# Kernel optimization log

Hardware: AMD Instinct MI355X
Metric: run time of the kernel (lower is better)

The kernel has to match this reference:

```python
import jax, jax.numpy as jnp
import numpy as np

D = 9  # nodefeat_n1 = 3 (resnet feat) + 6 (pos)


def _lstm_scan(x, Wih, Whh, bih, bhh, reverse=False):
    # x: [T, B, D] -> hidden states [T, B, D]; torch gate order i,f,g,o
    B = x.shape[1]
    def step(carry, xt):
        h, c = carry
        g = xt @ Wih.T + bih + h @ Whh.T + bhh
        i = jax.nn.sigmoid(g[:, :D])
        f = jax.nn.sigmoid(g[:, D:2*D])
        gg = jnp.tanh(g[:, 2*D:3*D])
        o = jax.nn.sigmoid(g[:, 3*D:])
        c = f * c + i * gg
        h = o * jnp.tanh(c)
        return (h, c), h
    init = (jnp.zeros((B, D), x.dtype), jnp.zeros((B, D), x.dtype))
    _, hs = jax.lax.scan(step, init, x, reverse=reverse)
    return hs


def _forward(nodes_feature, pos, attmat, msg_W, msg_b, gru_Wih, gru_Whh, gru_bih, gru_bhh,
             ro1_W, ro1_b, ro2_W, ro2_b, lf_Wih, lf_Whh, lf_bih, lf_bhh,
             lb_Wih, lb_Whh, lb_bih, lb_bhh, lr1_W, lr1_b, lr2_W, lr2_b, num_rec):
    node_feat = jnp.concatenate([nodes_feature, pos], axis=-1)  # [N,T,M,D]
    N, T, M, _ = node_feat.shape
    # valid_node_num = num_rec[b, 0] in the original code
    valid = (jnp.arange(M)[None, :] < num_rec[:, 0:1]).astype(node_feat.dtype)  # [N,M]
    att = attmat * valid[:, None, None, :]  # zero out invalid source nodes q
    src = node_feat  # message sources (h_w)
    hv = node_feat   # GRU hidden (h_v)
    hidden = node_feat
    for _ in range(2):  # iterN = 2 message-passing rounds
        msg = src @ msg_W.T + msg_b                    # [N,T,M,D] message_fc
        m = jnp.einsum('btnq,btqd->btnd', att, msg)    # attention-weighted sum over q
        # single-step GRU cell (torch gate order r,z,n)
        gx = m @ gru_Wih.T + gru_bih
        gh = hv @ gru_Whh.T + gru_bhh
        r = jax.nn.sigmoid(gx[..., :D] + gh[..., :D])
        z = jax.nn.sigmoid(gx[..., D:2*D] + gh[..., D:2*D])
        n = jnp.tanh(gx[..., 2*D:] + r * gh[..., 2*D:])
        h_new = (1.0 - z) * n + z * hv
        hidden = h_new * valid[:, None, :, None]       # invalid nodes never updated -> stay zero
        src = hidden
        hv = hidden
    vmask = valid[:, None, :, None]
    # per-frame readout (pred_label0)
    p0 = jax.nn.relu(hidden @ ro1_W.T + ro1_b) @ ro2_W.T + ro2_b
    pred_label0 = p0 * vmask
    # bidirectional LSTM over time, batched over (batch, node)
    x = hidden.transpose(1, 0, 2, 3).reshape(T, N * M, D)  # [T, N*M, D]
    hf = _lstm_scan(x, lf_Wih, lf_Whh, lf_bih, lf_bhh, reverse=False)
    hb = _lstm_scan(x, lb_Wih, lb_Whh, lb_bih, lb_bhh, reverse=True)
    out = jnp.concatenate([hf, hb], axis=-1).reshape(T, N, M, 2 * D).transpose(1, 0, 2, 3)
    p = jax.nn.relu(out @ lr1_W.T + lr1_b) @ lr2_W.T + lr2_b
    pred_label = p * vmask
    return pred_label, pred_label0


def setup_inputs() -> dict:
    key = jax.random.key(0)
    ks = jax.random.split(key, 32)
    N, T, M = 8192, 20, 6
    def u(k, shape, fan_in):
        s = 1.0 / np.sqrt(fan_in).astype(np.float32)
        return jax.random.uniform(k, shape, jnp.float32, -s, s)
    return {
        "nodes_feature": jax.random.normal(ks[0], (N, T, M, 3), jnp.float32),
        "pos": jax.random.normal(ks[1], (N, T, M, 6), jnp.float32),
        "attmat": jax.random.uniform(ks[2], (N, T, M, M), jnp.float32),
        "msg_W": u(ks[3], (D, D), D), "msg_b": u(ks[4], (D,), D),
        "gru_Wih": u(ks[5], (3 * D, D), D), "gru_Whh": u(ks[6], (3 * D, D), D),
        "gru_bih": u(ks[7], (3 * D,), D), "gru_bhh": u(ks[8], (3 * D,), D),
        "ro1_W": u(ks[9], (D, D), D), "ro1_b": u(ks[10], (D,), D),
        "ro2_W": u(ks[11], (7, D), D), "ro2_b": u(ks[12], (7,), D),
        "lf_Wih": u(ks[13], (4 * D, D), D), "lf_Whh": u(ks[14], (4 * D, D), D),
        "lf_bih": u(ks[15], (4 * D,), D), "lf_bhh": u(ks[16], (4 * D,), D),
        "lb_Wih": u(ks[17], (4 * D, D), D), "lb_Whh": u(ks[18], (4 * D, D), D),
        "lb_bih": u(ks[19], (4 * D,), D), "lb_bhh": u(ks[20], (4 * D,), D),
        "lr1_W": u(ks[21], (D, 2 * D), 2 * D), "lr1_b": u(ks[22], (D,), 2 * D),
        "lr2_W": u(ks[23], (7, D), D), "lr2_b": u(ks[24], (7,), D),
        "num_rec": jax.random.randint(ks[25], (N, T), 1, M + 1),
    }


def reference(nodes_feature, pos, attmat, msg_W, msg_b, gru_Wih, gru_Whh, gru_bih, gru_bhh,
              ro1_W, ro1_b, ro2_W, ro2_b, lf_Wih, lf_Whh, lf_bih, lf_bhh,
              lb_Wih, lb_Whh, lb_bih, lb_bhh, lr1_W, lr1_b, lr2_W, lr2_b, num_rec):
    return _forward(nodes_feature, pos, attmat, msg_W, msg_b, gru_Wih, gru_Whh, gru_bih, gru_bhh,
                    ro1_W, ro1_b, ro2_W, ro2_b, lf_Wih, lf_Whh, lf_bih, lf_bhh,
                    lb_Wih, lb_Whh, lb_bih, lb_bhh, lr1_W, lr1_b, lr2_W, lr2_b, num_rec)
```

## Files before the change

kernel.cpp:

```cpp
#include <hip/hip_runtime.h>

#define N_    8192
#define T_    20
#define M_    6
#define D_    9
#define NM_   (N_*M_)
#define NT_   (N_*T_)
#define NTM7_ (N_*T_*M_*7)

#define LOG2E 1.44269504088896f

__device__ __forceinline__ float sigm(float x){
    return __builtin_amdgcn_rcpf(1.f + __builtin_amdgcn_exp2f(-LOG2E * x));
}
__device__ __forceinline__ float tanh_(float x){
    return fmaf(2.f, __builtin_amdgcn_rcpf(1.f + __builtin_amdgcn_exp2f(-2.f*LOG2E * x)), -1.f);
}
__device__ __forceinline__ float shfl_(float v, int src){ return __shfl(v, src, 64); }

__global__ __launch_bounds__(256) void k_gnn(
    const float* __restrict__ nf,
    const float* __restrict__ pos,
    const float* __restrict__ am,
    const float* __restrict__ msgW, const float* __restrict__ msgb,
    const float* __restrict__ gWih, const float* __restrict__ gWhh,
    const float* __restrict__ gbih, const float* __restrict__ gbhh,
    const float* __restrict__ ro1W, const float* __restrict__ ro1b,
    const float* __restrict__ ro2W, const float* __restrict__ ro2b,
    const int*   __restrict__ numrec,
    float* __restrict__ hid,
    float* __restrict__ out0)
{
    const int lane = threadIdx.x & 63;
    const int wib  = threadIdx.x >> 6;
    const int g    = lane / 6;
    const int i    = lane - g * 6;
    const int gbase = g * 6;
    const bool lactive = (lane < 60);

    int ntIdx = (blockIdx.x * 4 + wib) * 10 + g;
    const bool active = lactive && (ntIdx < NT_);
    const int nt = active ? ntIdx : 0;
    const int n  = nt / T_;
    const int t  = nt - n * T_;

    float s[D_];
    {
        const float* p = nf + (size_t)nt * 18 + i * 3;
        s[0] = p[0]; s[1] = p[1]; s[2] = p[2];
    }
    {
        const float* p = pos + (size_t)nt * 36 + i * 6;
        #pragma unroll
        for (int k = 0; k < 6; ++k) s[3 + k] = p[k];
    }
    float attr[M_];
    {
        const float* p = am + (size_t)nt * 36 + i * 6;
        #pragma unroll
        for (int q = 0; q < M_; ++q) attr[q] = p[q];
    }
    const int nr = numrec[n * T_];
    #pragma unroll
    for (int q = 0; q < M_; ++q) attr[q] *= (q < nr) ? 1.f : 0.f;
    const float vmi = (i < nr) ? 1.f : 0.f;

    #pragma unroll
    for (int it = 0; it < 2; ++it) {
        float msg[D_];
        #pragma unroll
        for (int d = 0; d < D_; ++d) {
            float a = msgb[d];
            #pragma unroll
            for (int k = 0; k < D_; ++k) a += s[k] * msgW[d*9 + k];
            msg[d] = a;
        }
        float mm[D_];
        #pragma unroll
        for (int d = 0; d < D_; ++d) {
            float a = 0.f;
            #pragma unroll
            for (int q = 0; q < M_; ++q) a += attr[q] * shfl_(msg[d], gbase + q);
            mm[d] = a;
        }
        float gx[27], gh[27];
        #pragma unroll
        for (int j = 0; j < 27; ++j) {
            float ax = gbih[j], ah = gbhh[j];
            #pragma unroll
            for (int k = 0; k < D_; ++k) {
                ax += mm[k] * gWih[j*9 + k];
                ah += s[k]  * gWhh[j*9 + k];
            }
            gx[j] = ax; gh[j] = ah;
        }
        #pragma unroll
        for (int d = 0; d < D_; ++d) {
            float r  = sigm(gx[d]       + gh[d]);
            float z  = sigm(gx[9 + d]   + gh[9 + d]);
            float nn = tanh_(gx[18 + d] + r * gh[18 + d]);
            s[d] = vmi * ((1.f - z) * nn + z * s[d]);
        }
    }

    if (active) {
        float* hp = hid + (size_t)(n * M_ + i) * (T_ * D_) + t * D_;
        #pragma unroll
        for (int d = 0; d < D_; ++d) hp[d] = s[d];
    }

    float q9[D_];
    #pragma unroll
    for (int d = 0; d < D_; ++d) {
        float a = ro1b[d];
        #pragma unroll
        for (int k = 0; k < D_; ++k) a += s[k] * ro1W[d*9 + k];
        q9[d] = fmaxf(a, 0.f);
    }
    if (active) {
        float* op = out0 + (size_t)nt * 42 + i * 7;
        #pragma unroll
        for (int j = 0; j < 7; ++j) {
            float a = ro2b[j];
            #pragma unroll
            for (int k = 0; k < D_; ++k) a += q9[k] * ro2W[j*9 + k];
            op[j] = a * vmi;
        }
    }
}

#define CPB 14

__global__ __launch_bounds__(128) void k_lstm(
    const float* __restrict__ hid,
    const float* __restrict__ fWih, const float* __restrict__ fWhh,
    const float* __restrict__ fbih, const float* __restrict__ fbhh,
    const float* __restrict__ bWih, const float* __restrict__ bWhh,
    const float* __restrict__ bbih, const float* __restrict__ bbhh,
    const float* __restrict__ lr1W, const float* __restrict__ lr1b,
    const float* __restrict__ lr2W, const float* __restrict__ lr2b,
    const int*   __restrict__ numrec,
    float* __restrict__ out)
{
    __shared__ float hst[16 * 404];
    __shared__ float hxs[16 * 20];

    const int lane = threadIdx.x & 63;
    const int wib  = threadIdx.x >> 6;
    const int grp0 = lane / 9;
    const int d    = lane - grp0 * 9;
    const int row  = wib * 8 + grp0;
    const int grp  = (grp0 < 7) ? grp0 : 6;

    bool active = (lane < 63);
    int ci = blockIdx.x * CPB + wib * 7 + grp;
    active = active && (ci < NM_);
    const int nm = active ? ci : 0;

    const float* xb = hid + (size_t)nm * (T_ * D_);
    const int crow = row * 20;
    const int hrow = row * 404;

    {
        float wxi[9], wxf[9], wxg[9], wxo[9], whi[9], whf[9], whg[9], who[9];
        #pragma unroll
        for (int k = 0; k < 9; ++k) {
            wxi[k] = fWih[(d     )*9 + k];  whi[k] = fWhh[(d     )*9 + k];
            wxf[k] = fWih[(9  + d)*9 + k];  whf[k] = fWhh[(9  + d)*9 + k];
            wxg[k] = fWih[(18 + d)*9 + k];  whg[k] = fWhh[(18 + d)*9 + k];
            wxo[k] = fWih[(27 + d)*9 + k];  who[k] = fWhh[(27 + d)*9 + k];
        }
        const float bi = fbih[d]      + fbhh[d];
        const float bf = fbih[9 + d]  + fbhh[9 + d];
        const float bg = fbih[18 + d] + fbhh[18 + d];
        const float bo = fbih[27 + d] + fbhh[27 + d];

        hxs[crow + 2*d] = 0.f;
        float h = 0.f, c = 0.f;
        for (int t = 0; t < T_; ++t) {
            hxs[crow + 2*d + 1] = xb[t*9 + d];
            float gi = bi, gf = bf, gg = bg, go = bo;
            #pragma unroll
            for (int j = 0; j < 8; j += 2) {
                float4 v = *(const float4*)&hxs[crow + 2*j];
                gi = fmaf(v.x, whi[j], fmaf(v.y, wxi[j], gi));
                gf = fmaf(v.x, whf[j], fmaf(v.y, wxf[j], gf));
                gg = fmaf(v.x, whg[j], fmaf(v.y, wxg[j], gg));
                go = fmaf(v.x, who[j], fmaf(v.y, wxo[j], go));
                gi = fmaf(v.z, whi[j+1], fmaf(v.w, wxi[j+1], gi));
                gf = fmaf(v.z, whf[j+1], fmaf(v.w, wxf[j+1], gf));
                gg = fmaf(v.z, whg[j+1], fmaf(v.w, wxg[j+1], gg));
                go = fmaf(v.z, who[j+1], fmaf(v.w, wxo[j+1], go));
            }
            {
                float2 v = *(const float2*)&hxs[crow + 16];
                gi = fmaf(v.x, whi[8], fmaf(v.y, wxi[8], gi));
                gf = fmaf(v.x, whf[8], fmaf(v.y, wxf[8], gf));
                gg = fmaf(v.x, whg[8], fmaf(v.y, wxg[8], gg));
                go = fmaf(v.x, who[8], fmaf(v.y, wxo[8], go));
            }
            c = sigm(gf) * c + sigm(gi) * tanh_(gg);
            h = sigm(go) * tanh_(c);
            hst[hrow + t*20 + d] = h;
            hxs[crow + 2*d] = h;
        }
    }

    {
        float wxi[9], wxf[9], wxg[9], wxo[9], whi[9], whf[9], whg[9], who[9];
        #pragma unroll
        for (int k = 0; k < 9; ++k) {
            wxi[k] = bWih[(d     )*9 + k];  whi[k] = bWhh[(d     )*9 + k];
            wxf[k] = bWih[(9  + d)*9 + k];  whf[k] = bWhh[(9  + d)*9 + k];
            wxg[k] = bWih[(18 + d)*9 + k];  whg[k] = bWhh[(18 + d)*9 + k];
            wxo[k] = bWih[(27 + d)*9 + k];  who[k] = bWhh[(27 + d)*9 + k];
        }
        const float bi = bbih[d]      + bbhh[d];
        const float bf = bbih[9 + d]  + bbhh[9 + d];
        const float bg = bbih[18 + d] + bbhh[18 + d];
        const float bo = bbih[27 + d] + bbhh[27 + d];

        hxs[crow + 2*d] = 0.f;
        float h = 0.f, c = 0.f;
        for (int tt = T_ - 1; tt >= 0; --tt) {
            hxs[crow + 2*d + 1] = xb[tt*9 + d];
            float gi = bi, gf = bf, gg = bg, go = bo;
            #pragma unroll
            for (int j = 0; j < 8; j += 2) {
                float4 v = *(const float4*)&hxs[crow + 2*j];
                gi = fmaf(v.x, whi[j], fmaf(v.y, wxi[j], gi));
                gf = fmaf(v.x, whf[j], fmaf(v.y, wxf[j], gf));
                gg = fmaf(v.x, whg[j], fmaf(v.y, wxg[j], gg));
                go = fmaf(v.x, who[j], fmaf(v.y, wxo[j], go));
                gi = fmaf(v.z, whi[j+1], fmaf(v.w, wxi[j+1], gi));
                gf = fmaf(v.z, whf[j+1], fmaf(v.w, wxf[j+1], gf));
                gg = fmaf(v.z, whg[j+1], fmaf(v.w, wxg[j+1], gg));
                go = fmaf(v.z, who[j+1], fmaf(v.w, wxo[j+1], go));
            }
            {
                float2 v = *(const float2*)&hxs[crow + 16];
                gi = fmaf(v.x, whi[8], fmaf(v.y, wxi[8], gi));
                gf = fmaf(v.x, whf[8], fmaf(v.y, wxf[8], gf));
                gg = fmaf(v.x, whg[8], fmaf(v.y, wxg[8], gg));
                go = fmaf(v.x, who[8], fmaf(v.y, wxo[8], go));
            }
            c = sigm(gf) * c + sigm(gi) * tanh_(gg);
            h = sigm(go) * tanh_(c);
            hst[hrow + tt*20 + 10 + d] = h;
            hxs[crow + 2*d] = h;
        }
    }

    #pragma unroll 1
    for (int rr = 0; rr < 3; ++rr) {
        const int item = rr * 64 + lane;
        if (item >= 140) break;
        const int ch = item / 20;
        const int t  = item - ch * 20;
        const int ci2 = blockIdx.x * CPB + wib * 7 + ch;
        if (ci2 >= NM_) continue;
        const int base = (wib * 8 + ch) * 404 + t * 20;

        float hf[9], hb[9];
        #pragma unroll
        for (int j = 0; j < 4; ++j) {
            float2 a = *(const float2*)&hst[base + 2*j];
            hf[2*j] = a.x; hf[2*j+1] = a.y;
            float2 b = *(const float2*)&hst[base + 10 + 2*j];
            hb[2*j] = b.x; hb[2*j+1] = b.y;
        }
        hf[8] = hst[base + 8];
        hb[8] = hst[base + 18];

        const int n2 = ci2 / M_;
        const int m2 = ci2 - n2 * M_;
        const float vi = (m2 < numrec[n2 * T_]) ? 1.f : 0.f;

        float q[9];
        #pragma unroll
        for (int dd = 0; dd < 9; ++dd) {
            float a = lr1b[dd];
            #pragma unroll
            for (int k = 0; k < 9; ++k) a = fmaf(hf[k], lr1W[dd*18 + k], a);
            #pragma unroll
            for (int k = 0; k < 9; ++k) a = fmaf(hb[k], lr1W[dd*18 + 9 + k], a);
            q[dd] = fmaxf(a, 0.f);
        }
        float* op = out + (size_t)((n2 * T_ + t) * M_ + m2) * 7;
        #pragma unroll
        for (int j = 0; j < 7; ++j) {
            float a = lr2b[j];
            #pragma unroll
            for (int k = 0; k < 9; ++k) a = fmaf(q[k], lr2W[j*9 + k], a);
            op[j] = a * vi;
        }
    }
}

extern "C" void kernel_launch(void* const* d_in, const int* in_sizes, int n_in,
                              void* d_out, int out_size, void* d_ws, size_t ws_size,
                              hipStream_t stream) {
    const float* nf    = (const float*)d_in[0];
    const float* pos   = (const float*)d_in[1];
    const float* am    = (const float*)d_in[2];
    const float* msgW  = (const float*)d_in[3];
    const float* msgb  = (const float*)d_in[4];
    const float* gWih  = (const float*)d_in[5];
    const float* gWhh  = (const float*)d_in[6];
    const float* gbih  = (const float*)d_in[7];
    const float* gbhh  = (const float*)d_in[8];
    const float* ro1W  = (const float*)d_in[9];
    const float* ro1b  = (const float*)d_in[10];
    const float* ro2W  = (const float*)d_in[11];
    const float* ro2b  = (const float*)d_in[12];
    const float* lfWih = (const float*)d_in[13];
    const float* lfWhh = (const float*)d_in[14];
    const float* lfbih = (const float*)d_in[15];
    const float* lfbhh = (const float*)d_in[16];
    const float* lbWih = (const float*)d_in[17];
    const float* lbWhh = (const float*)d_in[18];
    const float* lbbih = (const float*)d_in[19];
    const float* lbbhh = (const float*)d_in[20];
    const float* lr1W  = (const float*)d_in[21];
    const float* lr1b  = (const float*)d_in[22];
    const float* lr2W  = (const float*)d_in[23];
    const float* lr2b  = (const float*)d_in[24];
    const int* numrec  = (const int*)d_in[25];

    float* hid = (float*)d_ws;

    float* outp = (float*)d_out;
    float* out0 = (float*)d_out + NTM7_;

    k_gnn <<<NT_ / 40, 256, 0, stream>>>(nf, pos, am, msgW, msgb, gWih, gWhh,
                                         gbih, gbhh, ro1W, ro1b, ro2W, ro2b,
                                         numrec, hid, out0);
    const int lgrid = (NM_ + CPB - 1) / CPB;
    k_lstm<<<lgrid, 128, 0, stream>>>(hid, lfWih, lfWhh, lfbih, lfbhh,
                                      lbWih, lbWhh, lbbih, lbbhh,
                                      lr1W, lr1b, lr2W, lr2b, numrec, outp);
}
```

Measured before the change: 329.7 us.

## Process two (n,t) groups per lane in GNN kernel using packed float2 math

Each lane in the GNN kernel now handles two frame groups at once, holding state as two-wide float vectors so the compiler can emit packed FP32 FMA instructions, and the grid is halved to match. The r and z gate biases and matmuls are also merged into one accumulator, which removes separate gx/gh arrays for those gates. The aim is to cut ALU instruction count and amortise the scalar weight loads over twice the work. In exchange, register pressure rises and occupancy may drop, and the bounds guard against NT_ is removed, which relies on NT_ being a multiple of 80.

```diff
diff --git a/kernel.cpp b/kernel.cpp
--- a/kernel.cpp
+++ b/kernel.cpp
@@ -10,6 +10,8 @@
 
 #define LOG2E 1.44269504088896f
 
+typedef __attribute__((ext_vector_type(2))) float v2f;
+
 __device__ __forceinline__ float sigm(float x){
     return __builtin_amdgcn_rcpf(1.f + __builtin_amdgcn_exp2f(-LOG2E * x));
 }
@@ -17,6 +19,13 @@
     return fmaf(2.f, __builtin_amdgcn_rcpf(1.f + __builtin_amdgcn_exp2f(-2.f*LOG2E * x)), -1.f);
 }
 __device__ __forceinline__ float shfl_(float v, int src){ return __shfl(v, src, 64); }
+__device__ __forceinline__ v2f splat(float s){ return (v2f){s, s}; }
+__device__ __forceinline__ v2f shfl2(v2f v, int src){
+    v2f r; r.x = __shfl(v.x, src, 64); r.y = __shfl(v.y, src, 64); return r;
+}
+__device__ __forceinline__ v2f sigm2(v2f x){ v2f r; r.x = sigm(x.x); r.y = sigm(x.y); return r; }
+__device__ __forceinline__ v2f tanh2(v2f x){ v2f r; r.x = tanh_(x.x); r.y = tanh_(x.y); return r; }
+__device__ __forceinline__ v2f relu2(v2f x){ v2f r; r.x = fmaxf(x.x,0.f); r.y = fmaxf(x.y,0.f); return r; }
 
 __global__ __launch_bounds__(256) void k_gnn(
     const float* __restrict__ nf,
@@ -38,93 +47,114 @@
     const int gbase = g * 6;
     const bool lactive = (lane < 60);
 
-    int ntIdx = (blockIdx.x * 4 + wib) * 10 + g;
-    const bool active = lactive && (ntIdx < NT_);
-    const int nt = active ? ntIdx : 0;
-    const int n  = nt / T_;
-    const int t  = nt - n * T_;
-
-    float s[D_];
-    {
-        const float* p = nf + (size_t)nt * 18 + i * 3;
-        s[0] = p[0]; s[1] = p[1]; s[2] = p[2];
-    }
-    {
-        const float* p = pos + (size_t)nt * 36 + i * 6;
-        #pragma unroll
-        for (int k = 0; k < 6; ++k) s[3 + k] = p[k];
-    }
-    float attr[M_];
-    {
-        const float* p = am + (size_t)nt * 36 + i * 6;
-        #pragma unroll
-        for (int q = 0; q < M_; ++q) attr[q] = p[q];
-    }
-    const int nr = numrec[n * T_];
+    const int wbase = (blockIdx.x * 4 + wib) * 20;
+    const int ntA = wbase + g;
+    const int ntB = wbase + 10 + g;
+    const int nA = ntA / T_, tA = ntA - nA * T_;
+    const int nB = ntB / T_, tB = ntB - nB * T_;
+
+    v2f s[D_];
+    {
+        const float* pA = nf + (size_t)ntA * 18 + i * 3;
+        const float* pB = nf + (size_t)ntB * 18 + i * 3;
+        #pragma unroll
+        for (int k = 0; k < 3; ++k) { s[k].x = pA[k]; s[k].y = pB[k]; }
+    }
+    {
+        const float* pA = pos + (size_t)ntA * 36 + i * 6;
+        const float* pB = pos + (size_t)ntB * 36 + i * 6;
+        #pragma unroll
+        for (int k = 0; k < 6; ++k) { s[3+k].x = pA[k]; s[3+k].y = pB[k]; }
+    }
+    v2f attr[M_];
+    {
+        const float* pA = am + (size_t)ntA * 36 + i * 6;
+        const float* pB = am + (size_t)ntB * 36 + i * 6;
+        #pragma unroll
+        for (int q = 0; q < M_; ++q) { attr[q].x = pA[q]; attr[q].y = pB[q]; }
+    }
+    const int nrA = numrec[nA * T_];
+    const int nrB = numrec[nB * T_];
     #pragma unroll
-    for (int q = 0; q < M_; ++q) attr[q] *= (q < nr) ? 1.f : 0.f;
-    const float vmi = (i < nr) ? 1.f : 0.f;
+    for (int q = 0; q < M_; ++q) {
+        attr[q].x *= (q < nrA) ? 1.f : 0.f;
+        attr[q].y *= (q < nrB) ? 1.f : 0.f;
+    }
+    v2f vmi; vmi.x = (i < nrA) ? 1.f : 0.f; vmi.y = (i < nrB) ? 1.f : 0.f;
 
     #pragma unroll
     for (int it = 0; it < 2; ++it) {
-        float msg[D_];
+        v2f msg[D_];
         #pragma unroll
         for (int d = 0; d < D_; ++d) {
-            float a = msgb[d];
+            v2f a = splat(msgb[d]);
             #pragma unroll
             for (int k = 0; k < D_; ++k) a += s[k] * msgW[d*9 + k];
             msg[d] = a;
         }
-        float mm[D_];
+        v2f mm[D_];
         #pragma unroll
         for (int d = 0; d < D_; ++d) {
-            float a = 0.f;
-            #pragma unroll
-            for (int q = 0; q < M_; ++q) a += attr[q] * shfl_(msg[d], gbase + q);
+            v2f a = splat(0.f);
+            #pragma unroll
+            for (int q = 0; q < M_; ++q) a += attr[q] * shfl2(msg[d], gbase + q);
             mm[d] = a;
         }
-        float gx[27], gh[27];
-        #pragma unroll
-        for (int j = 0; j < 27; ++j) {
-            float ax = gbih[j], ah = gbhh[j];
+        v2f grz[18], gxn[9], ghn[9];
+        #pragma unroll
+        for (int j = 0; j < 18; ++j) {
+            v2f a = splat(gbih[j] + gbhh[j]);
             #pragma unroll
             for (int k = 0; k < D_; ++k) {
-                ax += mm[k] * gWih[j*9 + k];
-                ah += s[k]  * gWhh[j*9 + k];
-            }
-            gx[j] = ax; gh[j] = ah;
+                a += mm[k] * gWih[j*9 + k];
+                a += s[k]  * gWhh[j*9 + k];
+            }
+            grz[j] = a;
+        }
+        #pragma unroll
+        for (int j = 0; j < 9; ++j) {
+            v2f ax = splat(gbih[18 + j]), ah = splat(gbhh[18 + j]);
+            #pragma unroll
+            for (int k = 0; k < D_; ++k) {
+                ax += mm[k] * gWih[(18 + j)*9 + k];
+                ah += s[k]  * gWhh[(18 + j)*9 + k];
+            }
+            gxn[j] = ax; ghn[j] = ah;
         }
         #pragma unroll
         for (int d = 0; d < D_; ++d) {
-            float r  = sigm(gx[d]       + gh[d]);
-            float z  = sigm(gx[9 + d]   + gh[9 + d]);
-            float nn = tanh_(gx[18 + d] + r * gh[18 + d]);
-            s[d] = vmi * ((1.f - z) * nn + z * s[d]);
-        }
-    }
-
-    if (active) {
-        float* hp = hid + (size_t)(n * M_ + i) * (T_ * D_) + t * D_;
-        #pragma unroll
-        for (int d = 0; d < D_; ++d) hp[d] = s[d];
-    }
-
-    float q9[D_];
+            v2f r  = sigm2(grz[d]);
+            v2f z  = sigm2(grz[9 + d]);
+            v2f nn = tanh2(gxn[d] + r * ghn[d]);
+            s[d] = vmi * ((splat(1.f) - z) * nn + z * s[d]);
+        }
+    }
+
+    if (lactive) {
+        float* hpA = hid + (size_t)(nA * M_ + i) * (T_ * D_) + tA * D_;
+        float* hpB = hid + (size_t)(nB * M_ + i) * (T_ * D_) + tB * D_;
+        #pragma unroll
+        for (int d = 0; d < D_; ++d) { hpA[d] = s[d].x; hpB[d] = s[d].y; }
+    }
+
+    v2f q9[D_];
     #pragma unroll
     for (int d = 0; d < D_; ++d) {
-        float a = ro1b[d];
+        v2f a = splat(ro1b[d]);
         #pragma unroll
         for (int k = 0; k < D_; ++k) a += s[k] * ro1W[d*9 + k];
-        q9[d] = fmaxf(a, 0.f);
-    }
-    if (active) {
-        float* op = out0 + (size_t)nt * 42 + i * 7;
+        q9[d] = relu2(a);
+    }
+    if (lactive) {
+        float* opA = out0 + (size_t)ntA * 42 + i * 7;
+        float* opB = out0 + (size_t)ntB * 42 + i * 7;
         #pragma unroll
         for (int j = 0; j < 7; ++j) {
-            float a = ro2b[j];
+            v2f a = splat(ro2b[j]);
             #pragma unroll
             for (int k = 0; k < D_; ++k) a += q9[k] * ro2W[j*9 + k];
-            op[j] = a * vmi;
+            a *= vmi;
+            opA[j] = a.x; opB[j] = a.y;
         }
     }
 }
@@ -332,7 +362,7 @@
     float* outp = (float*)d_out;
     float* out0 = (float*)d_out + NTM7_;
 
-    k_gnn <<<NT_ / 40, 256, 0, stream>>>(nf, pos, am, msgW, msgb, gWih, gWhh,
+    k_gnn <<<NT_ / 80, 256, 0, stream>>>(nf, pos, am, msgW, msgb, gWih, gWhh,
                                          gbih, gbhh, ro1W, ro1b, ro2W, ro2b,
                                          numrec, hid, out0);
     const int lgrid = (NM_ + CPB - 1) / CPB;
```

Result: faster. 323.2 us (-2.0%).
